# Kernel tuning notes

Measured on AMD Instinct MI355X. Metric: run time of the kernel, lower is better.

Reference implementation:

```python
import jax, jax.numpy as jnp
import numpy as np

D = 2048          # hidden_size
N = 16            # num query heads
K = 8             # num kv heads
G = N // K        # GQA groups
H = 128           # head_dim (== head_dim_original, already padded)
T_NOISE = 1024
T_PAD = 1024
MAX_KV = 4096
THETA = 1000000.0
EPS = 1e-6
SM_SCALE = H ** -0.5
NEG = -1e30


def apply_rope(x, pos):
    # x: (T, heads, H); rotate-half (NeoX/Qwen) convention over full head_dim
    half = H // 2
    inv_freq = 1.0 / (THETA ** (jnp.arange(half, dtype=jnp.float32) / half))
    ang = pos.astype(jnp.float32)[:, None] * inv_freq[None, :]      # (T, half)
    cos = jnp.cos(ang)[:, None, :]
    sin = jnp.sin(ang)[:, None, :]
    x1, x2 = x[..., :half], x[..., half:]
    return jnp.concatenate([x1 * cos - x2 * sin, x2 * cos + x1 * sin], axis=-1)


def rms_norm(x, scale):
    var = jnp.mean(jnp.square(x), axis=-1, keepdims=True)
    return x * jax.lax.rsqrt(var + EPS) * scale


def setup_inputs() -> dict:
    key = jax.random.key(0)
    ks = jax.random.split(key, 10)
    cache_len = 1024
    actual_ctx = 768
    u = lambda k, shape: jax.random.uniform(k, shape, jnp.float32) * 0.01  # nnx uniform init
    return {
        "x_noise": jax.random.normal(ks[0], (T_NOISE, D), jnp.float32),
        "target_hidden": jax.random.normal(ks[1], (T_PAD, D), jnp.float32),
        "noise_positions": jnp.arange(T_NOISE, dtype=jnp.int32) + cache_len + actual_ctx,
        "ctx_positions": jnp.arange(T_PAD, dtype=jnp.int32) + cache_len,
        "kv_cache_k": jax.random.normal(ks[2], (1, N, MAX_KV, H), jnp.float32),
        "kv_cache_v": jax.random.normal(ks[3], (1, N, MAX_KV, H), jnp.float32),
        "cache_len": cache_len,
        "actual_ctx_count": actual_ctx,
        "Wq": u(ks[4], (D, N, H)),
        "Wk": u(ks[5], (D, K, H)),
        "Wv": u(ks[6], (D, K, H)),
        "Wo": u(ks[7], (N, H, D)),
        "q_scale": u(ks[8], (H,)),
        "k_scale": u(ks[9], (H,)),
    }


def reference(x_noise, target_hidden, noise_positions, ctx_positions,
              kv_cache_k, kv_cache_v, cache_len, actual_ctx_count,
              Wq, Wk, Wv, Wo, q_scale, k_scale):
    T_noise = x_noise.shape[0]
    T_padded = target_hidden.shape[0]
    # Q projection + RMSNorm + RoPE
    q = jnp.einsum('td,dnh->tnh', x_noise, Wq)
    q = apply_rope(rms_norm(q, q_scale), noise_positions)              # (Tq, N, H)
    # K/V over [context, noise]
    x_new = jnp.concatenate([target_hidden, x_noise], axis=0)
    k_new = jnp.einsum('td,dkh->tkh', x_new, Wk)
    v_new = jnp.einsum('td,dkh->tkh', x_new, Wv)
    new_positions = jnp.concatenate([ctx_positions, noise_positions], axis=0)
    k_new = apply_rope(rms_norm(k_new, k_scale), new_positions)
    # GQA expand before cache write (matches original)
    if G > 1:
        k_new = jnp.repeat(k_new, G, axis=1)
        v_new = jnp.repeat(v_new, G, axis=1)
    # Phase A: masked context write at cache_len
    ctx_mask = (jnp.arange(T_padded) < actual_ctx_count)[:, None, None]
    k_ctx = jnp.where(ctx_mask, k_new[:T_padded], 0.0)
    v_ctx = jnp.where(ctx_mask, v_new[:T_padded], 0.0)
    to4d = lambda a: a.transpose(1, 0, 2)[None]                        # (1, N, T, H)
    kv_cache_k = jax.lax.dynamic_update_slice(kv_cache_k, to4d(k_ctx), (0, 0, cache_len, 0))
    kv_cache_v = jax.lax.dynamic_update_slice(kv_cache_v, to4d(v_ctx), (0, 0, cache_len, 0))
    # Phase B: noise write at cache_len + actual_ctx_count
    noise_start = cache_len + actual_ctx_count
    kv_cache_k = jax.lax.dynamic_update_slice(kv_cache_k, to4d(k_new[T_padded:]), (0, 0, noise_start, 0))
    kv_cache_v = jax.lax.dynamic_update_slice(kv_cache_v, to4d(v_new[T_padded:]), (0, 0, noise_start, 0))
    new_cache_len = noise_start + T_noise
    # Non-causal attention over full cache, padding masked (segment_ids semantics)
    kv_valid = jnp.arange(MAX_KV) < new_cache_len                      # (MAX_KV,)
    scores = jnp.einsum('qnh,nkh->nqk', q, kv_cache_k[0]) * SM_SCALE   # (N, Tq, MAX_KV)
    scores = jnp.where(kv_valid[None, None, :], scores, NEG)
    probs = jax.nn.softmax(scores, axis=-1)
    attn = jnp.einsum('nqk,nkh->qnh', probs, kv_cache_v[0])            # (Tq, N, H)
    output = jnp.einsum('qnh,nhd->qd', attn, Wo)                       # (Tq, D)
    return (output, kv_cache_k, kv_cache_v)
```

## Files before the change

### kernel.cpp

```cpp
#include <hip/hip_runtime.h>
#include <hip/hip_bf16.h>
#include <math.h>

#define D 2048
#define NH 16
#define KHD 8
#define HD 128
#define T_NOISE 1024
#define T_PAD 1024
#define MAX_KV 4096
#define SM_SCALE 0.08838834764831845f

typedef __attribute__((ext_vector_type(8))) short short8;
typedef __attribute__((ext_vector_type(4))) short short4v;
typedef __attribute__((ext_vector_type(4))) float f32x4;

__device__ __forceinline__ unsigned short f2bf(float f) {
    union { float f; unsigned u; } v; v.f = f;
    unsigned r = v.u + 0x7fff + ((v.u >> 16) & 1);
    return (unsigned short)(r >> 16);
}
__device__ __forceinline__ float bf2f(short s) {
    union { unsigned u; float f; } v; v.u = ((unsigned)(unsigned short)s) << 16;
    return v.f;
}
__device__ __forceinline__ void gload16(const void* g, void* l) {
    __builtin_amdgcn_global_load_lds(
        (const __attribute__((address_space(1))) unsigned int*)g,
        (__attribute__((address_space(3))) unsigned int*)l, 16, 0, 0);
}
__device__ __forceinline__ unsigned cvtpk(float lo, float hi) {
    unsigned r;
    asm("v_cvt_pk_bf16_f32 %0, %1, %2" : "=v"(r) : "v"(lo), "v"(hi));
    return r;
}

__global__ __launch_bounds__(256)
void cast_concat(const float* __restrict__ A0, const float* __restrict__ A1,
                 short* __restrict__ out, int splitElems) {
    int i = (blockIdx.x * 256 + threadIdx.x) * 8;
    const float* src = (i < splitElems) ? (A0 + i) : (A1 + (i - splitElems));
    float4 f0 = *(const float4*)src;
    float4 f1 = *(const float4*)(src + 4);
    short8 s;
    s[0] = (short)f2bf(f0.x); s[1] = (short)f2bf(f0.y);
    s[2] = (short)f2bf(f0.z); s[3] = (short)f2bf(f0.w);
    s[4] = (short)f2bf(f1.x); s[5] = (short)f2bf(f1.y);
    s[6] = (short)f2bf(f1.z); s[7] = (short)f2bf(f1.w);
    *(short8*)(out + i) = s;
}

__global__ __launch_bounds__(256)
void conv_transpose(const float* __restrict__ W, short* __restrict__ Wt,
                    int R, int C) {
    __shared__ short t[64][72];
    int tid = threadIdx.x;
    int r0 = blockIdx.y * 64, c0 = blockIdx.x * 64;
    int rl = tid >> 4, cl4 = (tid & 15) * 4;
    #pragma unroll
    for (int j = 0; j < 4; ++j) {
        int r = rl + j * 16;
        float4 f = *(const float4*)(W + (size_t)(r0 + r) * C + c0 + cl4);
        t[cl4 + 0][r] = (short)f2bf(f.x);
        t[cl4 + 1][r] = (short)f2bf(f.y);
        t[cl4 + 2][r] = (short)f2bf(f.z);
        t[cl4 + 3][r] = (short)f2bf(f.w);
    }
    __syncthreads();
    #pragma unroll
    for (int j = 0; j < 2; ++j) {
        int idx = tid + j * 256;
        int cr = idx >> 3, rc8 = (idx & 7) * 8;
        *(short8*)(Wt + (size_t)(c0 + cr) * R + r0 + rc8) = *(const short8*)&t[cr][rc8];
    }
}

__global__ __launch_bounds__(256)
void gemm_qkv64(const short* __restrict__ xbf, const short* __restrict__ Btp,
                short* __restrict__ k_tmpb, short* __restrict__ v_tmpb,
                short* __restrict__ q_tmpb) {
    const int n0 = blockIdx.x * 128;
    const int m0 = blockIdx.y * 64;
    const bool isQ = (n0 >= 2048);
    if (isQ && m0 >= 1024) return;
    const short* A = xbf + (isQ ? (size_t)1024 * 2048 : 0);

    __shared__ __align__(16) short As[64 * 32];
    __shared__ __align__(16) short Bs[128 * 32];
    const int tid = threadIdx.x;
    const int w = tid >> 6, lane = tid & 63;
    const int g = lane >> 4, li = lane & 15;
    const int wr = w >> 1, wc = w & 1;

    f32x4 acc[2][4];
    #pragma unroll
    for (int mi = 0; mi < 2; ++mi)
        #pragma unroll
        for (int ni = 0; ni < 4; ++ni) {
            acc[mi][ni][0] = 0.f; acc[mi][ni][1] = 0.f;
            acc[mi][ni][2] = 0.f; acc[mi][ni][3] = 0.f;
        }

    for (int k0 = 0; k0 < 2048; k0 += 32) {
        {
            int idx = w * 64 + lane;
            int row = idx >> 2, slot = idx & 3;
            gload16(A + (size_t)(m0 + row) * 2048 + k0 + slot * 8,
                    (char*)As + (size_t)(w * 64) * 16);
        }
        #pragma unroll
        for (int i = 0; i < 2; ++i) {
            int idx = i * 256 + w * 64 + lane;
            int row = idx >> 2, slot = idx & 3;
            gload16(Btp + (size_t)(n0 + row) * 2048 + k0 + slot * 8,
                    (char*)Bs + (size_t)(i * 256 + w * 64) * 16);
        }
        __syncthreads();
        short8 af[2], bf[4];
        #pragma unroll
        for (int mi = 0; mi < 2; ++mi)
            af[mi] = *(const short8*)&As[(wr * 32 + mi * 16 + li) * 32 + g * 8];
        #pragma unroll
        for (int ni = 0; ni < 4; ++ni)
            bf[ni] = *(const short8*)&Bs[(wc * 64 + ni * 16 + li) * 32 + g * 8];
        #pragma unroll
        for (int mi = 0; mi < 2; ++mi)
            #pragma unroll
            for (int ni = 0; ni < 4; ++ni)
                acc[mi][ni] = __builtin_amdgcn_mfma_f32_16x16x32_bf16(
                    af[mi], bf[ni], acc[mi][ni], 0, 0, 0);
        __syncthreads();
    }
    short* cp; int cbase, ldc2;
    if (n0 < 1024)      { cp = k_tmpb; cbase = 0;    ldc2 = 1024; }
    else if (n0 < 2048) { cp = v_tmpb; cbase = 1024; ldc2 = 1024; }
    else                { cp = q_tmpb; cbase = 2048; ldc2 = 2048; }
    #pragma unroll
    for (int mi = 0; mi < 2; ++mi)
        #pragma unroll
        for (int ni = 0; ni < 4; ++ni) {
            int n = n0 + wc * 64 + ni * 16 + li - cbase;
            #pragma unroll
            for (int r = 0; r < 4; ++r) {
                int m = m0 + wr * 32 + mi * 16 + 4 * g + r;
                cp[(size_t)m * ldc2 + n] = (short)f2bf(acc[mi][ni][r]);
            }
        }
}

__global__ __launch_bounds__(256)
void gemm_bf16_64(const short* __restrict__ A, const short* __restrict__ Bt,
                  float* __restrict__ C, int ldc, int K) {
    __shared__ __align__(16) short As[64 * 32];
    __shared__ __align__(16) short Bs[128 * 32];
    const int tid = threadIdx.x;
    const int w = tid >> 6, lane = tid & 63;
    const int g = lane >> 4, li = lane & 15;
    const int wr = w >> 1, wc = w & 1;
    const int m0 = blockIdx.y * 64, n0 = blockIdx.x * 128;

    f32x4 acc[2][4];
    #pragma unroll
    for (int mi = 0; mi < 2; ++mi)
        #pragma unroll
        for (int ni = 0; ni < 4; ++ni) {
            acc[mi][ni][0] = 0.f; acc[mi][ni][1] = 0.f;
            acc[mi][ni][2] = 0.f; acc[mi][ni][3] = 0.f;
        }

    for (int k0 = 0; k0 < K; k0 += 32) {
        {
            int idx = w * 64 + lane;
            int row = idx >> 2, slot = idx & 3;
            gload16(A + (size_t)(m0 + row) * K + k0 + slot * 8,
                    (char*)As + (size_t)(w * 64) * 16);
        }
        #pragma unroll
        for (int i = 0; i < 2; ++i) {
            int idx = i * 256 + w * 64 + lane;
            int row = idx >> 2, slot = idx & 3;
            gload16(Bt + (size_t)(n0 + row) * K + k0 + slot * 8,
                    (char*)Bs + (size_t)(i * 256 + w * 64) * 16);
        }
        __syncthreads();
        short8 af[2], bf[4];
        #pragma unroll
        for (int mi = 0; mi < 2; ++mi)
            af[mi] = *(const short8*)&As[(wr * 32 + mi * 16 + li) * 32 + g * 8];
        #pragma unroll
        for (int ni = 0; ni < 4; ++ni)
            bf[ni] = *(const short8*)&Bs[(wc * 64 + ni * 16 + li) * 32 + g * 8];
        #pragma unroll
        for (int mi = 0; mi < 2; ++mi)
            #pragma unroll
            for (int ni = 0; ni < 4; ++ni)
                acc[mi][ni] = __builtin_amdgcn_mfma_f32_16x16x32_bf16(
                    af[mi], bf[ni], acc[mi][ni], 0, 0, 0);
        __syncthreads();
    }
    #pragma unroll
    for (int mi = 0; mi < 2; ++mi)
        #pragma unroll
        for (int ni = 0; ni < 4; ++ni) {
            int n = n0 + wc * 64 + ni * 16 + li;
            #pragma unroll
            for (int r = 0; r < 4; ++r) {
                int m = m0 + wr * 32 + mi * 16 + 4 * g + r;
                C[(size_t)m * ldc + n] = acc[mi][ni][r];
            }
        }
}

__global__ __launch_bounds__(128)
void rmsrope_bf(short* __restrict__ x, int hpt,
                const int* __restrict__ posA, const int* __restrict__ posB,
                int splitT, const float* __restrict__ scale, float post) {
    __shared__ float red[128];
    __shared__ float nrm[128];
    int row = blockIdx.x;
    int h = threadIdx.x;
    float v = bf2f(x[(size_t)row * HD + h]);
    red[h] = v * v;
    __syncthreads();
    #pragma unroll
    for (int off = 64; off > 0; off >>= 1) {
        if (h < off) red[h] += red[h + off];
        __syncthreads();
    }
    float inv = rsqrtf(red[0] * (1.0f / 128.0f) + 1e-6f);
    nrm[h] = v * inv * scale[h];
    __syncthreads();
    if (h < 64) {
        int t = row / hpt;
        int pos = (t < splitT) ? posA[t] : posB[t - splitT];
        float inv_freq = expf((float)h * (-13.815510557964274f / 64.0f));
        float ang = (float)pos * inv_freq;
        float c = cosf(ang), s = sinf(ang);
        float x1 = nrm[h], x2 = nrm[h + 64];
        x[(size_t)row * HD + h]      = (short)f2bf((x1 * c - x2 * s) * post);
        x[(size_t)row * HD + h + 64] = (short)f2bf((x2 * c + x1 * s) * post);
    }
}

__global__ __launch_bounds__(256)
void cache_scatter2(const float* __restrict__ in_k, const float* __restrict__ in_v,
                    const short* __restrict__ k_tmpb, const short* __restrict__ v_tmpb,
                    float* __restrict__ out_k, float* __restrict__ out_v,
                    short* __restrict__ kbf, short* __restrict__ vbf,
                    const int* __restrict__ clp, const int* __restrict__ acp) {
    const int cache_len = clp[0], actx = acp[0];
    const int noise_start = cache_len + actx;
    const int new_len = noise_start + T_NOISE;
    int i = blockIdx.x * 256 + threadIdx.x;
    int n = i >> 16;
    int rem = i & 65535;
    int pos = rem >> 4;
    int h8 = (rem & 15) << 3;
    size_t co = ((size_t)(n * MAX_KV + pos)) * HD + h8;
    short8 ks8, vs8;
    if (pos >= cache_len && pos < new_len) {
        int tkn = (pos < noise_start) ? (pos - cache_len) : (T_PAD + (pos - noise_start));
        size_t so = ((size_t)(tkn * KHD + (n >> 1))) * HD + h8;
        ks8 = *(const short8*)(k_tmpb + so);
        vs8 = *(const short8*)(v_tmpb + so);
        float4 a, b;
        a.x = bf2f(ks8[0]); a.y = bf2f(ks8[1]); a.z = bf2f(ks8[2]); a.w = bf2f(ks8[3]);
        b.x = bf2f(ks8[4]); b.y = bf2f(ks8[5]); b.z = bf2f(ks8[6]); b.w = bf2f(ks8[7]);
        *(float4*)(out_k + co) = a; *(float4*)(out_k + co + 4) = b;
        a.x = bf2f(vs8[0]); a.y = bf2f(vs8[1]); a.z = bf2f(vs8[2]); a.w = bf2f(vs8[3]);
        b.x = bf2f(vs8[4]); b.y = bf2f(vs8[5]); b.z = bf2f(vs8[6]); b.w = bf2f(vs8[7]);
        *(float4*)(out_v + co) = a; *(float4*)(out_v + co + 4) = b;
    } else {
        float4 ka = *(const float4*)(in_k + co);
        float4 kb = *(const float4*)(in_k + co + 4);
        float4 va = *(const float4*)(in_v + co);
        float4 vb = *(const float4*)(in_v + co + 4);
        *(float4*)(out_k + co) = ka; *(float4*)(out_k + co + 4) = kb;
        *(float4*)(out_v + co) = va; *(float4*)(out_v + co + 4) = vb;
        ks8[0] = (short)f2bf(ka.x); ks8[1] = (short)f2bf(ka.y);
        ks8[2] = (short)f2bf(ka.z); ks8[3] = (short)f2bf(ka.w);
        ks8[4] = (short)f2bf(kb.x); ks8[5] = (short)f2bf(kb.y);
        ks8[6] = (short)f2bf(kb.z); ks8[7] = (short)f2bf(kb.w);
        vs8[0] = (short)f2bf(va.x); vs8[1] = (short)f2bf(va.y);
        vs8[2] = (short)f2bf(va.z); vs8[3] = (short)f2bf(va.w);
        vs8[4] = (short)f2bf(vb.x); vs8[5] = (short)f2bf(vb.y);
        vs8[6] = (short)f2bf(vb.z); vs8[7] = (short)f2bf(vb.w);
    }
    *(short8*)(kbf + co) = ks8;
    *(short8*)(vbf + co) = vs8;
}

#define VBUF(b) ((b) * 16896)

__device__ __forceinline__ short4v tr_read(unsigned addr) {
    short4v d;
    asm volatile("ds_read_b64_tr_b16 %0, %1" : "=v"(d) : "v"(addr));
    return d;
}

__global__ __launch_bounds__(128, 2)
void attn_mfma(const short* __restrict__ qbf, const short* __restrict__ kbf,
               const short* __restrict__ vbf, short* __restrict__ opA,
               short* __restrict__ opB, float* __restrict__ mlpart,
               const int* __restrict__ clp, const int* __restrict__ acp) {
    __shared__ __align__(16) char smem[33792];
    const int tid  = threadIdx.x;
    const int w    = tid >> 6;
    const int lane = tid & 63;
    const int g    = lane >> 4;
    const int li   = lane & 15;
    const int bid  = blockIdx.x;
    const int head = 2 * (bid & 7) + ((bid >> 3) & 1);
    const int rest = bid >> 4;
    const int q0   = (rest & 15) * 64;
    const int kvs  = rest >> 4;
    const int new_len = clp[0] + acp[0] + T_NOISE;
    const int ntiles  = (new_len + 63) >> 6;
    const int ntq     = (ntiles + 3) >> 2;

    const short* kb_g = kbf + (size_t)head * MAX_KV * HD;
    const short* vb_g = vbf + (size_t)head * MAX_KV * HD;

    short8 qf[2][4];
    #pragma unroll
    for (int sub = 0; sub < 2; ++sub) {
        const short* qp = qbf + ((size_t)(q0 + w * 32 + sub * 16 + li) * NH + head) * HD;
        #pragma unroll
        for (int ks = 0; ks < 4; ++ks) qf[sub][ks] = *(const short8*)(qp + 32 * ks + 8 * g);
    }

    f32x4 acc[2][8];
    #pragma unroll
    for (int sub = 0; sub < 2; ++sub)
        #pragma unroll
        for (int n = 0; n < 8; ++n) {
            acc[sub][n][0] = 0.f; acc[sub][n][1] = 0.f;
            acc[sub][n][2] = 0.f; acc[sub][n][3] = 0.f;
        }
    float m[2], l[2];
    m[0] = -INFINITY; m[1] = -INFINITY; l[0] = 0.f; l[1] = 0.f;

    const int vrloc = 4 * (lane >> 3) + ((lane >> 1) & 3);
    const int vcof  = (lane & 1) * 8;

    auto STAGE = [&](int tt, int bb) {
        const int base = (kvs * ntq + tt) * 64;
        #pragma unroll
        for (int half = 0; half < 2; ++half)
            #pragma unroll
            for (int i2 = 0; i2 < 4; ++i2) {
                const int ht = w * 4 + i2;
                gload16(vb_g + ((size_t)(base + half * 32 + vrloc) << 7) + ht * 16 + vcof,
                        smem + VBUF(bb) + half * 8448 + ht * 1056);
            }
    };

    short8 kpre[16];
    auto KLOAD = [&](int tt) {
        const int kp0 = (kvs * ntq + tt) << 6;
        const short* kr = kb_g + ((size_t)(kp0 + li) << 7) + g * 8;
        #pragma unroll
        for (int ks = 0; ks < 4; ++ks)
            #pragma unroll
            for (int j = 0; j < 4; ++j)
                kpre[ks * 4 + j] = *(const short8*)(kr + (size_t)(j * 16) * HD + ks * 32);
    };

    auto mkfrag = [&](const float* pA, const float* pB) -> short8 {
        unsigned w0 = cvtpk(pA[0], pA[1]), w1 = cvtpk(pA[2], pA[3]);
        unsigned w2 = cvtpk(pB[0], pB[1]), w3 = cvtpk(pB[2], pB[3]);
        const bool lowg = (g < 2);
        unsigned a0 = lowg ? w2 : w0, a1 = lowg ? w3 : w1;
        unsigned r0 = __shfl_xor((int)a0, 32), r1 = __shfl_xor((int)a1, 32);
        unsigned o0 = lowg ? w0 : w2, o1 = lowg ? w1 : w3;
        const bool sendOwn = (g == 1 || g == 2);
        unsigned b0 = sendOwn ? o0 : r0, b1 = sendOwn ? o1 : r1;
        unsigned g0_ = __shfl_xor((int)b0, 16), g1_ = __shfl_xor((int)b1, 16);
        union { unsigned u[4]; short8 s; } pau;
        pau.u[0] = (g == 0) ? o0 : (g == 2) ? r0 : g0_;
        pau.u[1] = (g == 0) ? o1 : (g == 2) ? r1 : g1_;
        pau.u[2] = (g == 3) ? o0 : (g == 1) ? r0 : g0_;
        pau.u[3] = (g == 3) ? o1 : (g == 1) ? r1 : g1_;
        return pau.s;
    };

    KLOAD(0);
    STAGE(0, 0);
    __syncthreads();

    for (int t = 0; t < ntq; ++t) {
        const int b = t & 1;
        if (t + 1 < ntq) STAGE(t + 1, b ^ 1);
        const int pos0 = (kvs * ntq + t) << 6;
        f32x4 s[4][2];
        #pragma unroll
        for (int j = 0; j < 4; ++j)
            #pragma unroll
            for (int sub = 0; sub < 2; ++sub) {
                s[j][sub][0] = 0.f; s[j][sub][1] = 0.f;
                s[j][sub][2] = 0.f; s[j][sub][3] = 0.f;
            }
        #pragma unroll
        for (int ks = 0; ks < 4; ++ks)
            #pragma unroll
            for (int j = 0; j < 4; ++j) {
                short8 kf = kpre[ks * 4 + j];
                s[j][0] = __builtin_amdgcn_mfma_f32_16x16x32_bf16(kf, qf[0][ks], s[j][0], 0, 0, 0);
                s[j][1] = __builtin_amdgcn_mfma_f32_16x16x32_bf16(kf, qf[1][ks], s[j][1], 0, 0, 0);
            }
        if (t + 1 < ntq) KLOAD(t + 1);
        #pragma unroll
        for (int j = 0; j < 4; ++j)
            #pragma unroll
            for (int r = 0; r < 4; ++r)
                if (pos0 + 16 * j + 4 * g + r >= new_len) {
                    s[j][0][r] = -1e30f; s[j][1][r] = -1e30f;
                }
        short8 pa[2][2];
        #pragma unroll
        for (int sub = 0; sub < 2; ++sub) {
            float tm = -INFINITY;
            #pragma unroll
            for (int j = 0; j < 4; ++j)
                #pragma unroll
                for (int r = 0; r < 4; ++r) tm = fmaxf(tm, s[j][sub][r]);
            tm = fmaxf(tm, __shfl_xor(tm, 16));
            tm = fmaxf(tm, __shfl_xor(tm, 32));
            if (tm > m[sub] + 8.f) {
                const float alpha = __expf(m[sub] - tm);
                m[sub] = tm;
                l[sub] *= alpha;
                #pragma unroll
                for (int n = 0; n < 8; ++n) {
                    acc[sub][n][0] *= alpha; acc[sub][n][1] *= alpha;
                    acc[sub][n][2] *= alpha; acc[sub][n][3] *= alpha;
                }
            }
            const float mb = m[sub];
            float p[4][4];
            float rs = 0.f;
            #pragma unroll
            for (int j = 0; j < 4; ++j)
                #pragma unroll
                for (int r = 0; r < 4; ++r) {
                    p[j][r] = __expf(s[j][sub][r] - mb);
                    rs += p[j][r];
                }
            rs += __shfl_xor(rs, 16);
            rs += __shfl_xor(rs, 32);
            l[sub] += rs;
            pa[sub][0] = mkfrag(p[0], p[1]);
            pa[sub][1] = mkfrag(p[2], p[3]);
        }
        #pragma unroll
        for (int half = 0; half < 2; ++half) {
            const unsigned vb0 = (unsigned)(size_t)(smem + VBUF(b)) + half * 8448
                               + g * 256 + li * 8;
            short4v vt[16];
            #pragma unroll
            for (int h2 = 0; h2 < 8; ++h2) {
                vt[2 * h2]     = tr_read(vb0 + h2 * 1056);
                vt[2 * h2 + 1] = tr_read(vb0 + h2 * 1056 + 128);
            }
            asm volatile("s_waitcnt lgkmcnt(0)" ::: "memory");
            __builtin_amdgcn_sched_barrier(0);
            #pragma unroll
            for (int h2 = 0; h2 < 8; ++h2) {
                short8 vf = __builtin_shufflevector(vt[2 * h2], vt[2 * h2 + 1],
                                                    0, 1, 2, 3, 4, 5, 6, 7);
                acc[0][h2] = __builtin_amdgcn_mfma_f32_16x16x32_bf16(vf, pa[0][half], acc[0][h2], 0, 0, 0);
                acc[1][h2] = __builtin_amdgcn_mfma_f32_16x16x32_bf16(vf, pa[1][half], acc[1][h2], 0, 0, 0);
            }
        }
        __syncthreads();
    }

    short* op = (kvs < 2) ? (opA + (size_t)kvs * 16 * 1024 * 128)
                          : (opB + (size_t)(kvs - 2) * 16 * 1024 * 128);
    #pragma unroll
    for (int sub = 0; sub < 2; ++sub) {
        const int qrow = q0 + w * 32 + sub * 16 + li;
        const size_t ro = ((size_t)(head << 10) + qrow) * 128;
        #pragma unroll
        for (int n = 0; n < 8; ++n) {
            short4v o4;
            o4[0] = (short)f2bf(acc[sub][n][0]); o4[1] = (short)f2bf(acc[sub][n][1]);
            o4[2] = (short)f2bf(acc[sub][n][2]); o4[3] = (short)f2bf(acc[sub][n][3]);
            *(short4v*)(op + ro + 16 * n + 4 * g) = o4;
        }
        if (g == 0) {
            float* ml = mlpart + (((size_t)(kvs * 16 + head) << 10) + qrow) * 2;
            ml[0] = m[sub]; ml[1] = l[sub];
        }
    }
}

__global__ __launch_bounds__(256)
void attn_merge(const short* __restrict__ opA, const short* __restrict__ opB,
                const float* __restrict__ mlpart, short* __restrict__ a_bf) {
    int gid = blockIdx.x * 256 + threadIdx.x;
    int row = gid >> 4;
    int c8  = (gid & 15) * 8;
    int head = row >> 10, q = row & 1023;
    float mg[4], lg[4], mstar = -INFINITY;
    #pragma unroll
    for (int s = 0; s < 4; ++s) {
        const float* ml = mlpart + (((size_t)(s * 16 + head) << 10) + q) * 2;
        mg[s] = ml[0]; lg[s] = ml[1];
        mstar = fmaxf(mstar, mg[s]);
    }
    float cg[4], lstar = 0.f;
    #pragma unroll
    for (int s = 0; s < 4; ++s) { cg[s] = __expf(mg[s] - mstar); lstar += lg[s] * cg[s]; }
    const float inv = 1.0f / lstar;
    float o[8] = {};
    #pragma unroll
    for (int s = 0; s < 4; ++s) {
        const short* op = (s < 2) ? (opA + (size_t)s * 16 * 1024 * 128)
                                  : (opB + (size_t)(s - 2) * 16 * 1024 * 128);
        short8 v = *(const short8*)(op + (((size_t)(head << 10)) + q) * 128 + c8);
        #pragma unroll
        for (int j = 0; j < 8; ++j) o[j] += cg[s] * bf2f(v[j]);
    }
    short8 o8;
    #pragma unroll
    for (int j = 0; j < 8; ++j) o8[j] = (short)f2bf(o[j] * inv);
    *(short8*)(a_bf + (size_t)q * 2048 + head * 128 + c8) = o8;
}

extern "C" void kernel_launch(void* const* d_in, const int* in_sizes, int n_in,
                              void* d_out, int out_size, void* d_ws, size_t ws_size,
                              hipStream_t stream) {
    const float* x_noise       = (const float*)d_in[0];
    const float* target_hidden = (const float*)d_in[1];
    const int*   noise_pos     = (const int*)d_in[2];
    const int*   ctx_pos       = (const int*)d_in[3];
    const float* in_k          = (const float*)d_in[4];
    const float* in_v          = (const float*)d_in[5];
    const int*   clp           = (const int*)d_in[6];
    const int*   acp           = (const int*)d_in[7];
    const float* Wq            = (const float*)d_in[8];
    const float* Wk            = (const float*)d_in[9];
    const float* Wv            = (const float*)d_in[10];
    const float* Wo            = (const float*)d_in[11];
    const float* q_scale       = (const float*)d_in[12];
    const float* k_scale       = (const float*)d_in[13];

    float* out   = (float*)d_out;
    float* out_k = out + (size_t)T_NOISE * D;
    float* out_v = out_k + (size_t)NH * MAX_KV * HD;

    float* ws     = (float*)d_ws;
    const size_t M1 = 1024u * 1024u;
    short* q_tmpb = (short*)ws;
    short* a_bf   = q_tmpb;
    short* k_tmpb = (short*)(ws + 1 * M1);
    short* v_tmpb = (short*)(ws + 2 * M1);
    float* mlpart = (float*)v_tmpb;
    short* xbf    = (short*)(ws + 3 * M1);
    short* opartA = xbf;
    short* btpack = (short*)(ws + 5 * M1);
    short* wo_t   = btpack;
    short* opartB = (short*)(ws + 7 * M1);
    short* kbf    = (short*)(ws + 9 * M1);
    short* vbf    = (short*)(ws + 13 * M1);

    dim3 blk(256);
    cast_concat<<<2048, blk, 0, stream>>>(target_hidden, x_noise, xbf, 1024 * 2048);
    conv_transpose<<<dim3(16, 32), blk, 0, stream>>>(Wk, btpack, 2048, 1024);
    conv_transpose<<<dim3(16, 32), blk, 0, stream>>>(Wv, btpack + (size_t)1024 * 2048, 2048, 1024);
    conv_transpose<<<dim3(32, 32), blk, 0, stream>>>(Wq, btpack + (size_t)2048 * 2048, 2048, 2048);
    gemm_qkv64<<<dim3(32, 32), blk, 0, stream>>>(xbf, btpack, k_tmpb, v_tmpb, q_tmpb);
    conv_transpose<<<dim3(32, 32), blk, 0, stream>>>(Wo, wo_t, 2048, 2048);
    rmsrope_bf<<<1024 * 16, 128, 0, stream>>>(q_tmpb, NH, noise_pos, noise_pos, 2048,
                                              q_scale, SM_SCALE);
    rmsrope_bf<<<2048 * 8, 128, 0, stream>>>(k_tmpb, KHD, ctx_pos, noise_pos, 1024,
                                             k_scale, 1.0f);
    cache_scatter2<<<4096, blk, 0, stream>>>(in_k, in_v, k_tmpb, v_tmpb,
                                             out_k, out_v, kbf, vbf, clp, acp);
    attn_mfma<<<1024, 128, 0, stream>>>(q_tmpb, kbf, vbf, opartA, opartB, mlpart, clp, acp);
    attn_merge<<<1024, blk, 0, stream>>>(opartA, opartB, mlpart, a_bf);
    gemm_bf16_64<<<dim3(16, 16), blk, 0, stream>>>(a_bf, wo_t, out, 2048, 2048);
}
```

Measured before the change: 226.8 us.

## Split attention KV range six ways with single-buffered V staging

Raises the flash-decoding KV split from 4 to 6, launching 1536 attention blocks instead of 1024, and the merge kernel now combines six partial outputs. The V tile in LDS goes from double to single buffering, which halves shared memory and lets launch bounds request 3 blocks per CU. The cost is that V staging no longer overlaps compute, since each tile waits on a barrier. Partial-output buffers are reassigned across workspace regions and the output buffer, and out-of-range tiles are clamped or skipped.

```diff
diff --git a/kernel.cpp b/kernel.cpp
--- a/kernel.cpp
+++ b/kernel.cpp
@@ -9,6 +9,7 @@
 #define T_NOISE 1024
 #define T_PAD 1024
 #define MAX_KV 4096
+#define NSPLIT 6
 #define SM_SCALE 0.08838834764831845f
 
 typedef __attribute__((ext_vector_type(8))) short short8;
@@ -290,20 +291,21 @@
     *(short8*)(vbf + co) = vs8;
 }
 
-#define VBUF(b) ((b) * 16896)
-
 __device__ __forceinline__ short4v tr_read(unsigned addr) {
     short4v d;
     asm volatile("ds_read_b64_tr_b16 %0, %1" : "=v"(d) : "v"(addr));
     return d;
 }
 
-__global__ __launch_bounds__(128, 2)
+__global__ __launch_bounds__(128, 3)
 void attn_mfma(const short* __restrict__ qbf, const short* __restrict__ kbf,
-               const short* __restrict__ vbf, short* __restrict__ opA,
-               short* __restrict__ opB, float* __restrict__ mlpart,
+               const short* __restrict__ vbf,
+               short* __restrict__ op0, short* __restrict__ op1,
+               short* __restrict__ op2, short* __restrict__ op3,
+               short* __restrict__ op4, short* __restrict__ op5,
+               float* __restrict__ mlpart,
                const int* __restrict__ clp, const int* __restrict__ acp) {
-    __shared__ __align__(16) char smem[33792];
+    __shared__ __align__(16) char smem[16896];
     const int tid  = threadIdx.x;
     const int w    = tid >> 6;
     const int lane = tid & 63;
@@ -316,7 +318,7 @@
     const int kvs  = rest >> 4;
     const int new_len = clp[0] + acp[0] + T_NOISE;
     const int ntiles  = (new_len + 63) >> 6;
-    const int ntq     = (ntiles + 3) >> 2;
+    const int ntq     = (ntiles + NSPLIT - 1) / NSPLIT;
 
     const short* kb_g = kbf + (size_t)head * MAX_KV * HD;
     const short* vb_g = vbf + (size_t)head * MAX_KV * HD;
@@ -343,21 +345,23 @@
     const int vrloc = 4 * (lane >> 3) + ((lane >> 1) & 3);
     const int vcof  = (lane & 1) * 8;
 
-    auto STAGE = [&](int tt, int bb) {
-        const int base = (kvs * ntq + tt) * 64;
+    auto STAGE = [&](int tt) {
+        int base = (kvs * ntq + tt) * 64;
+        if (base > MAX_KV - 64) base = MAX_KV - 64;
         #pragma unroll
         for (int half = 0; half < 2; ++half)
             #pragma unroll
             for (int i2 = 0; i2 < 4; ++i2) {
                 const int ht = w * 4 + i2;
                 gload16(vb_g + ((size_t)(base + half * 32 + vrloc) << 7) + ht * 16 + vcof,
-                        smem + VBUF(bb) + half * 8448 + ht * 1056);
+                        smem + half * 8448 + ht * 1056);
             }
     };
 
     short8 kpre[16];
     auto KLOAD = [&](int tt) {
-        const int kp0 = (kvs * ntq + tt) << 6;
+        int kp0 = (kvs * ntq + tt) << 6;
+        if (kp0 > MAX_KV - 64) kp0 = MAX_KV - 64;
         const short* kr = kb_g + ((size_t)(kp0 + li) << 7) + g * 8;
         #pragma unroll
         for (int ks = 0; ks < 4; ++ks)
@@ -385,13 +389,11 @@
     };
 
     KLOAD(0);
-    STAGE(0, 0);
-    __syncthreads();
 
     for (int t = 0; t < ntq; ++t) {
-        const int b = t & 1;
-        if (t + 1 < ntq) STAGE(t + 1, b ^ 1);
         const int pos0 = (kvs * ntq + t) << 6;
+        if (pos0 >= new_len) break;
+        STAGE(t);
         f32x4 s[4][2];
         #pragma unroll
         for (int j = 0; j < 4; ++j)
@@ -452,9 +454,10 @@
             pa[sub][0] = mkfrag(p[0], p[1]);
             pa[sub][1] = mkfrag(p[2], p[3]);
         }
+        __syncthreads();
         #pragma unroll
         for (int half = 0; half < 2; ++half) {
-            const unsigned vb0 = (unsigned)(size_t)(smem + VBUF(b)) + half * 8448
+            const unsigned vb0 = (unsigned)(size_t)smem + half * 8448
                                + g * 256 + li * 8;
             short4v vt[16];
             #pragma unroll
@@ -475,8 +478,8 @@
         __syncthreads();
     }
 
-    short* op = (kvs < 2) ? (opA + (size_t)kvs * 16 * 1024 * 128)
-                          : (opB + (size_t)(kvs - 2) * 16 * 1024 * 128);
+    short* op = (kvs == 0) ? op0 : (kvs == 1) ? op1 : (kvs == 2) ? op2
+              : (kvs == 3) ? op3 : (kvs == 4) ? op4 : op5;
     #pragma unroll
     for (int sub = 0; sub < 2; ++sub) {
         const int qrow = q0 + w * 32 + sub * 16 + li;
@@ -496,29 +499,30 @@
 }
 
 __global__ __launch_bounds__(256)
-void attn_merge(const short* __restrict__ opA, const short* __restrict__ opB,
+void attn_merge(const short* __restrict__ op0, const short* __restrict__ op1,
+                const short* __restrict__ op2, const short* __restrict__ op3,
+                const short* __restrict__ op4, const short* __restrict__ op5,
                 const float* __restrict__ mlpart, short* __restrict__ a_bf) {
+    const short* ops[NSPLIT] = {op0, op1, op2, op3, op4, op5};
     int gid = blockIdx.x * 256 + threadIdx.x;
     int row = gid >> 4;
     int c8  = (gid & 15) * 8;
     int head = row >> 10, q = row & 1023;
-    float mg[4], lg[4], mstar = -INFINITY;
-    #pragma unroll
-    for (int s = 0; s < 4; ++s) {
+    float mg[NSPLIT], lg[NSPLIT], mstar = -INFINITY;
+    #pragma unroll
+    for (int s = 0; s < NSPLIT; ++s) {
         const float* ml = mlpart + (((size_t)(s * 16 + head) << 10) + q) * 2;
         mg[s] = ml[0]; lg[s] = ml[1];
         mstar = fmaxf(mstar, mg[s]);
     }
-    float cg[4], lstar = 0.f;
-    #pragma unroll
-    for (int s = 0; s < 4; ++s) { cg[s] = __expf(mg[s] - mstar); lstar += lg[s] * cg[s]; }
+    float cg[NSPLIT], lstar = 0.f;
+    #pragma unroll
+    for (int s = 0; s < NSPLIT; ++s) { cg[s] = __expf(mg[s] - mstar); lstar += lg[s] * cg[s]; }
     const float inv = 1.0f / lstar;
     float o[8] = {};
     #pragma unroll
-    for (int s = 0; s < 4; ++s) {
-        const short* op = (s < 2) ? (opA + (size_t)s * 16 * 1024 * 128)
-                                  : (opB + (size_t)(s - 2) * 16 * 1024 * 128);
-        short8 v = *(const short8*)(op + (((size_t)(head << 10)) + q) * 128 + c8);
+    for (int s = 0; s < NSPLIT; ++s) {
+        short8 v = *(const short8*)(ops[s] + (((size_t)(head << 10)) + q) * 128 + c8);
         #pragma unroll
         for (int j = 0; j < 8; ++j) o[j] += cg[s] * bf2f(v[j]);
     }
@@ -556,14 +560,18 @@
     short* a_bf   = q_tmpb;
     short* k_tmpb = (short*)(ws + 1 * M1);
     short* v_tmpb = (short*)(ws + 2 * M1);
-    float* mlpart = (float*)v_tmpb;
+    float* mlpart = (float*)(ws + 2 * M1);
     short* xbf    = (short*)(ws + 3 * M1);
-    short* opartA = xbf;
     short* btpack = (short*)(ws + 5 * M1);
     short* wo_t   = btpack;
-    short* opartB = (short*)(ws + 7 * M1);
     short* kbf    = (short*)(ws + 9 * M1);
     short* vbf    = (short*)(ws + 13 * M1);
+    short* op0 = k_tmpb;
+    short* op1 = xbf;
+    short* op2 = (short*)(ws + 4 * M1);
+    short* op3 = (short*)(ws + 7 * M1);
+    short* op4 = (short*)(ws + 8 * M1);
+    short* op5 = (short*)out;
 
     dim3 blk(256);
     cast_concat<<<2048, blk, 0, stream>>>(target_hidden, x_noise, xbf, 1024 * 2048);
@@ -578,7 +586,8 @@
                                              k_scale, 1.0f);
     cache_scatter2<<<4096, blk, 0, stream>>>(in_k, in_v, k_tmpb, v_tmpb,
                                              out_k, out_v, kbf, vbf, clp, acp);
-    attn_mfma<<<1024, 128, 0, stream>>>(q_tmpb, kbf, vbf, opartA, opartB, mlpart, clp, acp);
-    attn_merge<<<1024, blk, 0, stream>>>(opartA, opartB, mlpart, a_bf);
+    attn_mfma<<<16 * 16 * NSPLIT, 128, 0, stream>>>(
+        q_tmpb, kbf, vbf, op0, op1, op2, op3, op4, op5, mlpart, clp, acp);
+    attn_merge<<<1024, blk, 0, stream>>>(op0, op1, op2, op3, op4, op5, mlpart, a_bf);
     gemm_bf16_64<<<dim3(16, 16), blk, 0, stream>>>(a_bf, wo_t, out, 2048, 2048);
 }
```

Result: slower. 311.6 us (+37.4%).
